# Kernel optimization log

Hardware: AMD Instinct MI355X
Metric: run time of the kernel (lower is better)

## Reference

```python
import jax, jax.numpy as jnp
import numpy as np

EPS = 1e-6          # numerical floor for norms / denominators (fp32-safe)
PROJ_EPS = 1e-5     # ball projection margin: max norm = 1 - PROJ_EPS


def _norm(x):
    return jnp.sqrt(jnp.maximum(jnp.sum(x * x, axis=-1, keepdims=True), EPS * EPS))


def hyp_proj(x):
    # project onto open Poincare ball of radius 1 - PROJ_EPS
    n = _norm(x)
    scale = jnp.minimum((1.0 - PROJ_EPS) / n, 1.0)
    return x * scale


def exp_map_zero(v):
    n = _norm(v)
    return jnp.tanh(n) * v / n


def log_map_zero(y):
    n = _norm(y)
    return jnp.arctanh(jnp.minimum(n, 1.0 - PROJ_EPS)) * y / n


def mobius_add(x, y):
    x2 = jnp.sum(x * x, axis=-1, keepdims=True)
    y2 = jnp.sum(y * y, axis=-1, keepdims=True)
    xy = jnp.sum(x * y, axis=-1, keepdims=True)
    num = (1.0 + 2.0 * xy + y2) * x + (1.0 - x2) * y
    den = 1.0 + 2.0 * xy + x2 * y2
    return num / jnp.maximum(den, EPS)


def gcn_layer(x, rows, cols, vals, W, b, n_nodes, use_act):
    # tangent-space linear transform
    pre = log_map_zero(x)                      # [N, d]
    h = pre @ W                                # [N, d]
    # sparse adjacency matmul: agg[r] += val * h[c]
    msg = vals[:, None] * h[cols]              # [E, d]
    agg = jax.ops.segment_sum(msg, rows, num_segments=n_nodes)
    out = hyp_proj(exp_map_zero(agg))
    # hyperbolic bias via mobius addition
    bh = hyp_proj(exp_map_zero(b[None, :]))    # [1, d]
    out = hyp_proj(mobius_add(out, bh))
    if use_act:
        out = hyp_proj(exp_map_zero(jnp.tanh(log_map_zero(out))))
    return out


def setup_inputs() -> dict:
    key = jax.random.key(0)
    N, D, E = 100000, 64, 3200000
    ks = jax.random.split(key, 8)
    x = jax.random.normal(ks[0], (N, D), dtype=jnp.float32) * 0.1
    edge_vals = jax.random.uniform(ks[1], (E,), dtype=jnp.float32)
    W1 = jax.random.normal(ks[2], (D, D), dtype=jnp.float32) * (1.0 / np.sqrt(D))
    b1 = jnp.zeros((D,), dtype=jnp.float32)
    W2 = jax.random.normal(ks[3], (D, D), dtype=jnp.float32) * (1.0 / np.sqrt(D))
    b2 = jnp.zeros((D,), dtype=jnp.float32)
    edge_rows = jax.random.randint(ks[4], (E,), 0, N, dtype=jnp.int64 if jax.config.jax_enable_x64 else jnp.int32).astype(jnp.int32)
    edge_cols = jax.random.randint(ks[5], (E,), 0, N, dtype=jnp.int32)
    return {"x": x, "edge_vals": edge_vals, "W1": W1, "b1": b1,
            "W2": W2, "b2": b2, "edge_rows": edge_rows, "edge_cols": edge_cols}


def reference(x, edge_vals, W1, b1, W2, b2, edge_rows, edge_cols):
    n_nodes = x.shape[0]
    # HyperKA._graph_convolution: project base embeddings, then layers with
    # mobius residual; last layer has no activation.
    e0 = hyp_proj(x)
    h1 = gcn_layer(e0, edge_rows, edge_cols, edge_vals, W1, b1, n_nodes, use_act=True)
    h1 = hyp_proj(mobius_add(h1, e0))
    h2 = gcn_layer(h1, edge_rows, edge_cols, edge_vals, W2, b2, n_nodes, use_act=False)
    h2 = hyp_proj(mobius_add(h2, h1))
    return h2
```

## Files before the change

### kernel.cpp

```cpp
#include <hip/hip_runtime.h>
#include <math.h>

#define D 64
#define EPSF 1e-6f
#define EPS2F 1e-12f
#define PROJ_EPSF 1e-5f
#define EPB 16384

typedef _Float16 f16;
typedef f16 f16x4 __attribute__((ext_vector_type(4)));
typedef f16 f16x8 __attribute__((ext_vector_type(8)));
typedef float f32x4 __attribute__((ext_vector_type(4)));

__device__ __forceinline__ float frcp(float x)  { return __builtin_amdgcn_rcpf(x); }
__device__ __forceinline__ float fsqrt(float x) { return __builtin_amdgcn_sqrtf(x); }
__device__ __forceinline__ float ftanh(float x) {
    float e = __expf(2.0f * x);
    return (e - 1.0f) * frcp(e + 1.0f);
}
__device__ __forceinline__ float fatanh(float z) {
    return 0.5f * __logf((1.0f + z) * frcp(1.0f - z));
}

__device__ __forceinline__ float wave_sum(float v) {
#pragma unroll
    for (int o = 32; o > 0; o >>= 1) v += __shfl_xor(v, o, 64);
    return v;
}
__device__ __forceinline__ float qsum(float v) {
#pragma unroll
    for (int o = 1; o < 16; o <<= 1) v += __shfl_xor(v, o, 64);
    return v;
}

__global__ __launch_bounds__(256) void k1_hist_pre(
    const int* __restrict__ rows, const float* __restrict__ x,
    const float* __restrict__ b1, const float* __restrict__ b2,
    int* __restrict__ histT, f16* __restrict__ pre,
    float* __restrict__ nbuf, float* __restrict__ bhbuf,
    int E, int N, int nb1, int NBIN)
{
    const int bid = blockIdx.x, tid = threadIdx.x;
    const int lane = tid & 63;
    if (bid < nb1) {
        __shared__ int lh[512];
        for (int i = tid; i < NBIN; i += 256) lh[i] = 0;
        __syncthreads();
        const int e0 = bid * EPB;
#pragma unroll 4
        for (int k = 0; k < EPB / 256; ++k) {
            int e = e0 + k * 256 + tid;
            if (e < E) atomicAdd(&lh[__builtin_nontemporal_load(rows + e) >> 8], 1);
        }
        __syncthreads();
        for (int i = tid; i < NBIN; i += 256) histT[i * nb1 + bid] = lh[i];
    } else if (bid == nb1) {
        if (tid < 128) {
            int wsel = tid >> 6;
            const float* b = wsel ? b2 : b1;
            float bv = b[lane];
            float nb = fsqrt(fmaxf(wave_sum(bv * bv), EPS2F));
            float t = ftanh(nb);
            float v = bv * (t * frcp(nb));
            float nv = t;
            float sc = fminf((1.0f - PROJ_EPSF) * frcp(fmaxf(nv, EPSF)), 1.0f);
            v *= sc; nv = fminf(nv, 1.0f - PROJ_EPSF);
            bhbuf[wsel * 64 + lane] = v;
            if (lane == 0) bhbuf[128 + wsel] = nv;
        }
    } else {
        int node = (bid - nb1 - 1) * 4 + (tid >> 6);
        if (node >= N) return;
        float xv = x[(size_t)node * D + lane];
        float nx = fsqrt(fmaxf(wave_sum(xv * xv), EPS2F));
        float sc = fminf((1.0f - PROJ_EPSF) * frcp(nx), 1.0f);
        float e0 = xv * sc;
        float ne0 = fminf(nx, 1.0f - PROJ_EPSF);
        pre[(size_t)node * D + lane] = (f16)(e0 * (fatanh(ne0) * frcp(fmaxf(ne0, EPSF))));
        if (lane == 0) nbuf[node] = nx;
    }
}

__global__ __launch_bounds__(64) void scan_parts(int* __restrict__ part, int P)
{
    int lane = threadIdx.x;
    int carry = 0;
    for (int b = 0; b < P; b += 64) {
        int i = b + lane;
        int v = (i < P) ? part[i] : 0;
        int inc = v;
#pragma unroll
        for (int off = 1; off < 64; off <<= 1) {
            int tu = __shfl_up(inc, off, 64);
            if (lane >= off) inc += tu;
        }
        if (i < P) part[i] = inc - v + carry;
        carry += __shfl(inc, 63, 64);
    }
}

__global__ __launch_bounds__(256) void scan_apply(
    int* __restrict__ a, const int* __restrict__ part, int L)
{
    __shared__ int wbase[4];
    int t = threadIdx.x, lane = t & 63, wid = t >> 6;
    int idx0 = blockIdx.x * 1024 + t * 4;
    int v0 = 0, v1 = 0, v2 = 0, v3 = 0;
    if (idx0 < L) { int4 v = *(const int4*)(a + idx0); v0 = v.x; v1 = v.y; v2 = v.z; v3 = v.w; }
    int s = v0 + v1 + v2 + v3;
    int inc = s;
#pragma unroll
    for (int off = 1; off < 64; off <<= 1) {
        int tu = __shfl_up(inc, off, 64);
        if (lane >= off) inc += tu;
    }
    if (lane == 63) wbase[wid] = inc;
    __syncthreads();
    if (t == 0) { int acc = 0; for (int k = 0; k < 4; ++k) { int xx = wbase[k]; wbase[k] = acc; acc += xx; } }
    __syncthreads();
    int excl = part[blockIdx.x] + wbase[wid] + (inc - s);
    if (idx0 < L) {
        int4 o; o.x = excl; o.y = excl + v0; o.z = excl + v0 + v1; o.w = excl + v0 + v1 + v2;
        *(int4*)(a + idx0) = o;
    }
}

__global__ __launch_bounds__(256) void reduce_chunks(
    const int* __restrict__ src, int* __restrict__ part, int L)
{
    __shared__ int ws[4];
    const int tid = threadIdx.x, lane = tid & 63, wid4 = tid >> 6;
    int idx0 = blockIdx.x * 1024 + tid * 4;
    int s = 0;
    if (idx0 < L) { int4 v = *(const int4*)(src + idx0); s = v.x + v.y + v.z + v.w; }
    s = (int)wave_sum((float)s);
    if (lane == 0) ws[wid4] = s;
    __syncthreads();
    if (tid == 0) part[blockIdx.x] = ws[0] + ws[1] + ws[2] + ws[3];
}

__device__ __forceinline__ void gemm64_body(
    const f16* __restrict__ A, const float* __restrict__ W,
    f16* __restrict__ C, int M, int wid, int nwaves, int lane)
{
    const int m = lane & 15;
    const int quad = lane >> 4;
    f16x8 Bfr[2][4];
#pragma unroll
    for (int kt = 0; kt < 2; ++kt)
#pragma unroll
        for (int nt = 0; nt < 4; ++nt) {
            f16x8 tmp;
#pragma unroll
            for (int j = 0; j < 8; ++j)
                tmp[j] = (f16)W[(kt * 32 + quad * 8 + j) * D + nt * 16 + m];
            Bfr[kt][nt] = tmp;
        }
    const int ntile = M >> 4;
    for (int tile = wid; tile < ntile; tile += nwaves) {
        const f16* arow = A + (size_t)(tile * 16 + m) * D;
        f16x8 a0 = *(const f16x8*)(arow + quad * 8);
        f16x8 a1 = *(const f16x8*)(arow + 32 + quad * 8);
#pragma unroll
        for (int nt = 0; nt < 4; ++nt) {
            f32x4 z = {0.0f, 0.0f, 0.0f, 0.0f};
            z = __builtin_amdgcn_mfma_f32_16x16x32_f16(a0, Bfr[0][nt], z, 0, 0, 0);
            z = __builtin_amdgcn_mfma_f32_16x16x32_f16(a1, Bfr[1][nt], z, 0, 0, 0);
#pragma unroll
            for (int r = 0; r < 4; ++r)
                C[(size_t)(tile * 16 + quad * 4 + r) * D + nt * 16 + m] = (f16)z[r];
        }
    }
}

__global__ __launch_bounds__(256) void k2_reduce_gemm(
    const int* __restrict__ histT, int* __restrict__ part, int Lp, int P,
    const f16* __restrict__ A, const float* __restrict__ W,
    f16* __restrict__ C, int M)
{
    const int tid = threadIdx.x, lane = tid & 63, wid4 = tid >> 6;
    if ((int)blockIdx.x < P) {
        __shared__ int ws[4];
        int idx0 = blockIdx.x * 1024 + tid * 4;
        int s = 0;
        if (idx0 < Lp) { int4 v = *(const int4*)(histT + idx0); s = v.x + v.y + v.z + v.w; }
        s = (int)wave_sum((float)s);
        if (lane == 0) ws[wid4] = s;
        __syncthreads();
        if (tid == 0) part[blockIdx.x] = ws[0] + ws[1] + ws[2] + ws[3];
    } else {
        int wid = (blockIdx.x - P) * 4 + wid4;
        int nwaves = (gridDim.x - P) * 4;
        gemm64_body(A, W, C, M, wid, nwaves, lane);
    }
}

__global__ __launch_bounds__(512) void p1_scatter(
    const int* __restrict__ rows, const int* __restrict__ cols,
    const float* __restrict__ vals, const int* __restrict__ histT,
    unsigned int* __restrict__ pay, unsigned char* __restrict__ rloc,
    int E, int nb1, int NBIN)
{
    __shared__ unsigned int  stage[512][32];
    __shared__ unsigned char srloc[512][32];
    __shared__ int gbase[512];
    __shared__ int cnt[512];
    __shared__ int flushed[512];
    __shared__ unsigned int msk[512];

    const int bid = blockIdx.x, tid = threadIdx.x;
    {
        int i = tid;
        gbase[i] = (i < NBIN) ? histT[i * nb1 + bid] : 0;
        cnt[i] = 0; flushed[i] = 0; msk[i] = 0u;
    }
    __syncthreads();

    const int e0 = bid * EPB;
    for (int rnd = 0; rnd < EPB / 2048; ++rnd) {
        int rr[4], cc[4]; float vv[4];
#pragma unroll
        for (int u = 0; u < 4; ++u) {
            int e = e0 + rnd * 2048 + u * 512 + tid;
            bool ok = e < E;
            rr[u] = ok ? __builtin_nontemporal_load(rows + e) : -1;
            cc[u] = ok ? __builtin_nontemporal_load(cols + e) : 0;
            vv[u] = ok ? __builtin_nontemporal_load(vals + e) : 0.0f;
        }
#pragma unroll
        for (int u = 0; u < 4; ++u) {
            if (rr[u] < 0) continue;
            int bin = rr[u] >> 8;
            unsigned int q = (unsigned int)fmaf(vv[u], 32767.0f, 0.5f);
            unsigned int p = (q << 17) | (unsigned int)cc[u];
            unsigned char rl = (unsigned char)(rr[u] & 255);
            int slot = atomicAdd(&cnt[bin], 1);
            if (slot - flushed[bin] < 32) {
                stage[bin][slot & 31] = p;
                srloc[bin][slot & 31] = rl;
                atomicOr(&msk[bin], 1u << (slot & 31));
            } else {
                int gp = gbase[bin] + slot;
                pay[gp] = p;
                rloc[gp] = rl;
            }
        }
        __syncthreads();
        if (tid < NBIN) {
            const int b = tid;
            int f = flushed[b];
            int n = cnt[b];
            unsigned int m = msk[b];
            const int gb = gbase[b];
            while (n - f >= 16) {
                const int half = (f >> 4) & 1;
                const unsigned int m16 = (m >> (half * 16)) & 0xFFFFu;
                const int base = gb + f;
                const int r0 = half * 16;
                if (m16 == 0xFFFFu) {
#pragma unroll
                    for (int k2 = 0; k2 < 16; ++k2)
                        pay[base + k2] = stage[b][r0 + k2];
#pragma unroll
                    for (int k2 = 0; k2 < 16; ++k2)
                        rloc[base + k2] = srloc[b][r0 + k2];
                } else {
                    for (int k2 = 0; k2 < 16; ++k2)
                        if (m16 & (1u << k2)) {
                            pay[base + k2] = stage[b][r0 + k2];
                            rloc[base + k2] = srloc[b][r0 + k2];
                        }
                }
                m &= ~(0xFFFFu << (half * 16));
                f += 16;
            }
            flushed[b] = f;
            msk[b] = m;
        }
        __syncthreads();
    }
    if (tid < NBIN) {
        const int b = tid;
        int f = flushed[b];
        const int n = cnt[b];
        const unsigned int m = msk[b];
        const int gb = gbase[b];
        for (; f < n; ++f) {
            if (m & (1u << (f & 31))) {
                pay[gb + f] = stage[b][f & 31];
                rloc[gb + f] = srloc[b][f & 31];
            }
        }
    }
}

__global__ __launch_bounds__(256) void band_build(
    const unsigned int* __restrict__ pay, const unsigned char* __restrict__ rloc,
    const int* __restrict__ histT, int* __restrict__ rs,
    unsigned int* __restrict__ epack, int* __restrict__ dcnt,
    int E, int nb1, int NBIN, int N)
{
    __shared__ int lh[256];
    __shared__ int cur[256];
    __shared__ int dh[256];
    __shared__ int wsum[4];
    const int b = blockIdx.x, tid = threadIdx.x;
    const int lane = tid & 63, wid = tid >> 6;
    const int segstart = histT[b * nb1];
    const int segend = (b + 1 < NBIN) ? histT[(b + 1) * nb1] : E;
    lh[tid] = 0;
    dh[tid] = 0;
    __syncthreads();
    for (int j = segstart + tid; j < segend; j += 256)
        atomicAdd(&lh[rloc[j]], 1);
    __syncthreads();
    int v = lh[tid];
    int r = b * 256 + tid;
    if (r < N) atomicAdd(&dh[v > 255 ? 255 : v], 1);
    int inc = v;
#pragma unroll
    for (int off = 1; off < 64; off <<= 1) {
        int tu = __shfl_up(inc, off, 64);
        if (lane >= off) inc += tu;
    }
    if (lane == 63) wsum[wid] = inc;
    __syncthreads();
    int base = 0;
    for (int w2 = 0; w2 < wid; ++w2) base += wsum[w2];
    int excl = base + inc - v;
    cur[tid] = excl;
    if (r < N) rs[r] = segstart + excl + v;
    __syncthreads();
    dcnt[tid * NBIN + b] = dh[tid];
    for (int j = segstart + tid; j < segend; j += 256) {
        int pos = segstart + atomicAdd(&cur[rloc[j]], 1);
        epack[pos] = pay[j];
    }
}

__global__ __launch_bounds__(256) void perm_build(
    const int* __restrict__ rs, const int* __restrict__ dcnt,
    int* __restrict__ perm, int NBIN, int N)
{
    __shared__ int cur[256];
    const int b = blockIdx.x, tid = threadIdx.x;
    cur[tid] = dcnt[tid * NBIN + b];
    __syncthreads();
    int r = b * 256 + tid;
    if (r < N) {
        int d = rs[r] - (r ? rs[r - 1] : 0);
        if (d > 255) d = 255;
        int pos = atomicAdd(&cur[d], 1);
        perm[pos] = r;
    }
}

__device__ __forceinline__ void csr_accum4(
    const int* __restrict__ rs, const unsigned int* __restrict__ epack,
    const f16* __restrict__ h, int row, int li, int qbase, float* a)
{
    const int start = (row == 0) ? 0 : rs[row - 1];
    const int end = rs[row];
    int nbat = (end - start + 15) >> 4;
#pragma unroll
    for (int o = 16; o < 64; o <<= 1) {
        int nbo = __shfl_xor(nbat, o, 64);
        nbat = nbo > nbat ? nbo : nbat;
    }
    const f16x4* __restrict__ h4 = (const f16x4*)h;
    float A0[4] = {0.f, 0.f, 0.f, 0.f}, A1[4] = {0.f, 0.f, 0.f, 0.f};
    int j = start + li;
    unsigned int p = (j < end) ? epack[j] : 0u;
    for (int bb = 0; bb < nbat; ++bb) {
        int c = (int)(p & 131071u);
        float vf = (float)(p >> 17) * (1.0f / 32767.0f);
        int jn = j + 16;
        unsigned int pn = (jn < end) ? epack[jn] : 0u;
#pragma unroll
        for (int t = 0; t < 16; t += 4) {
            int   c0 = __shfl(c,  qbase + t,     64);
            float v0 = __shfl(vf, qbase + t,     64);
            int   c1 = __shfl(c,  qbase + t + 1, 64);
            float v1 = __shfl(vf, qbase + t + 1, 64);
            int   c2 = __shfl(c,  qbase + t + 2, 64);
            float v2 = __shfl(vf, qbase + t + 2, 64);
            int   c3 = __shfl(c,  qbase + t + 3, 64);
            float v3 = __shfl(vf, qbase + t + 3, 64);
            f16x4 h0 = h4[(size_t)c0 * 16 + li];
            f16x4 h1 = h4[(size_t)c1 * 16 + li];
            f16x4 h2 = h4[(size_t)c2 * 16 + li];
            f16x4 h3 = h4[(size_t)c3 * 16 + li];
#pragma unroll
            for (int k = 0; k < 4; ++k) {
                A0[k] = fmaf(v0, (float)h0[k], A0[k]);
                A1[k] = fmaf(v1, (float)h1[k], A1[k]);
                A0[k] = fmaf(v2, (float)h2[k], A0[k]);
                A1[k] = fmaf(v3, (float)h3[k], A1[k]);
            }
        }
        j = jn; p = pn;
    }
#pragma unroll
    for (int k = 0; k < 4; ++k) a[k] = A0[k] + A1[k];
}

__global__ __launch_bounds__(256) void layer1_fused(
    const int* __restrict__ rs, const unsigned int* __restrict__ epack,
    const f16* __restrict__ h, const float* __restrict__ x,
    const float* __restrict__ bhbuf, float* __restrict__ nbuf,
    const float* __restrict__ W2, const int* __restrict__ perm,
    f16* __restrict__ h1_out, f16* __restrict__ h2lin, int N)
{
    __shared__ f16 ptile[16 * 72];
    __shared__ f16 w2l[D * D];
    __shared__ int rowids[16];

    const int tid = threadIdx.x;
    const int lane = tid & 63;
    const int q = lane >> 4, li = lane & 15, qbase = q << 4;
    const int rb = (tid >> 6) * 4 + q;
    int prow = blockIdx.x * 16 + rb;
    if (prow >= N) prow = N - 1;
    const int row = perm[prow];

    {
        const float4* W4 = (const float4*)W2;
        int i = tid;
#pragma unroll
        for (int it = 0; it < 4; ++it, i += 256) {
            float4 v4 = W4[i];
            f16x4 c4 = {(f16)v4.x, (f16)v4.y, (f16)v4.z, (f16)v4.w};
            *(f16x4*)&w2l[i * 4] = c4;
        }
    }

    float a[4];
    csr_accum4(rs, epack, h, row, li, qbase, a);

    float na = fsqrt(fmaxf(qsum(a[0]*a[0] + a[1]*a[1] + a[2]*a[2] + a[3]*a[3]), EPS2F));
    float t = ftanh(na);
    float s = t * frcp(na);
    float o[4];
#pragma unroll
    for (int k = 0; k < 4; ++k) o[k] = a[k] * s;
    float no = t;
    float sc = fminf((1.0f - PROJ_EPSF) * frcp(fmaxf(no, EPSF)), 1.0f);
#pragma unroll
    for (int k = 0; k < 4; ++k) o[k] *= sc;
    no = fminf(no, 1.0f - PROJ_EPSF);

    float4 bp4 = ((const float4*)bhbuf)[li];
    float bh[4] = {bp4.x, bp4.y, bp4.z, bp4.w};
    float nbh = bhbuf[128];
    float xy = qsum(o[0]*bh[0] + o[1]*bh[1] + o[2]*bh[2] + o[3]*bh[3]);
    float x2 = no * no, y2 = nbh * nbh;
    float rd = frcp(fmaxf(1.0f + 2.0f * xy + x2 * y2, EPSF));
    float al = (1.0f + 2.0f * xy + y2) * rd;
    float be = (1.0f - x2) * rd;
    float m[4];
#pragma unroll
    for (int k = 0; k < 4; ++k) m[k] = al * o[k] + be * bh[k];
    float nm = fsqrt(fmaxf(al*al*x2 + be*be*y2 + 2.0f*al*be*xy, EPS2F));
    sc = fminf((1.0f - PROJ_EPSF) * frcp(fmaxf(nm, EPSF)), 1.0f);
#pragma unroll
    for (int k = 0; k < 4; ++k) m[k] *= sc;
    nm = fminf(nm, 1.0f - PROJ_EPSF);

    float lg = fatanh(nm) * frcp(fmaxf(nm, EPSF));
    float w[4];
#pragma unroll
    for (int k = 0; k < 4; ++k) w[k] = ftanh(m[k] * lg);
    float nw = fsqrt(fmaxf(qsum(w[0]*w[0] + w[1]*w[1] + w[2]*w[2] + w[3]*w[3]), EPS2F));
    float tw = ftanh(nw);
    s = tw * frcp(nw);
    float ov[4];
#pragma unroll
    for (int k = 0; k < 4; ++k) ov[k] = w[k] * s;
    float nov = tw;
    sc = fminf((1.0f - PROJ_EPSF) * frcp(fmaxf(nov, EPSF)), 1.0f);
#pragma unroll
    for (int k = 0; k < 4; ++k) ov[k] *= sc;
    nov = fminf(nov, 1.0f - PROJ_EPSF);

    float4 xp4 = ((const float4*)(x + (size_t)row * D))[li];
    float xp[4] = {xp4.x, xp4.y, xp4.z, xp4.w};
    float nx = nbuf[row];
    float sce = fminf((1.0f - PROJ_EPSF) * frcp(nx), 1.0f);
    float e0[4];
#pragma unroll
    for (int k = 0; k < 4; ++k) e0[k] = xp[k] * sce;
    float ne0 = fminf(nx, 1.0f - PROJ_EPSF);
    float xy2 = qsum(ov[0]*e0[0] + ov[1]*e0[1] + ov[2]*e0[2] + ov[3]*e0[3]);
    x2 = nov * nov; y2 = ne0 * ne0;
    rd = frcp(fmaxf(1.0f + 2.0f * xy2 + x2 * y2, EPSF));
    al = (1.0f + 2.0f * xy2 + y2) * rd;
    be = (1.0f - x2) * rd;
    float h1v[4];
#pragma unroll
    for (int k = 0; k < 4; ++k) h1v[k] = al * ov[k] + be * e0[k];
    float nh = fsqrt(fmaxf(al*al*x2 + be*be*y2 + 2.0f*al*be*xy2, EPS2F));
    sc = fminf((1.0f - PROJ_EPSF) * frcp(fmaxf(nh, EPSF)), 1.0f);
#pragma unroll
    for (int k = 0; k < 4; ++k) h1v[k] *= sc;
    nh = fminf(nh, 1.0f - PROJ_EPSF);

    f16x4 hp, pp;
    float lg2 = fatanh(nh) * frcp(fmaxf(nh, EPSF));
#pragma unroll
    for (int k = 0; k < 4; ++k) { hp[k] = (f16)h1v[k]; pp[k] = (f16)(h1v[k] * lg2); }
    ((f16x4*)h1_out)[(size_t)row * 16 + li] = hp;
    *(f16x4*)&ptile[rb * 72 + li * 4] = pp;
    if (li == 0) { rowids[rb] = row; nbuf[row] = nh; }
    __syncthreads();

    {
        const int wv = tid >> 6;
        f16x8 B2[2];
#pragma unroll
        for (int kt = 0; kt < 2; ++kt) {
            f16x8 tmp;
#pragma unroll
            for (int j = 0; j < 8; ++j)
                tmp[j] = w2l[(kt * 32 + q * 8 + j) * D + wv * 16 + li];
            B2[kt] = tmp;
        }
        f16x8 a0, a1;
#pragma unroll
        for (int j = 0; j < 8; ++j) {
            a0[j] = ptile[li * 72 + q * 8 + j];
            a1[j] = ptile[li * 72 + 32 + q * 8 + j];
        }
        f32x4 z = {0.0f, 0.0f, 0.0f, 0.0f};
        z = __builtin_amdgcn_mfma_f32_16x16x32_f16(a0, B2[0], z, 0, 0, 0);
        z = __builtin_amdgcn_mfma_f32_16x16x32_f16(a1, B2[1], z, 0, 0, 0);
#pragma unroll
        for (int r = 0; r < 4; ++r)
            h2lin[(size_t)rowids[q * 4 + r] * D + wv * 16 + li] = (f16)z[r];
    }
}

__global__ __launch_bounds__(256) void layer2_fused(
    const int* __restrict__ rs, const unsigned int* __restrict__ epack,
    const f16* __restrict__ h2lin, const float* __restrict__ bhbuf,
    const float* __restrict__ nbuf, const int* __restrict__ perm,
    f16* __restrict__ h1_inout, int N)
{
    const int tid = threadIdx.x;
    const int lane = tid & 63;
    const int q = lane >> 4, li = lane & 15, qbase = q << 4;
    const int rb = (tid >> 6) * 4 + q;
    int prow = blockIdx.x * 16 + rb;
    if (prow >= N) prow = N - 1;
    const int row = perm[prow];

    float a[4];
    csr_accum4(rs, epack, h2lin, row, li, qbase, a);

    float na = fsqrt(fmaxf(qsum(a[0]*a[0] + a[1]*a[1] + a[2]*a[2] + a[3]*a[3]), EPS2F));
    float t = ftanh(na);
    float s = t * frcp(na);
    float o[4];
#pragma unroll
    for (int k = 0; k < 4; ++k) o[k] = a[k] * s;
    float no = t;
    float sc = fminf((1.0f - PROJ_EPSF) * frcp(fmaxf(no, EPSF)), 1.0f);
#pragma unroll
    for (int k = 0; k < 4; ++k) o[k] *= sc;
    no = fminf(no, 1.0f - PROJ_EPSF);

    float4 bp4 = ((const float4*)(bhbuf + 64))[li];
    float bh[4] = {bp4.x, bp4.y, bp4.z, bp4.w};
    float nbh = bhbuf[129];
    float xy = qsum(o[0]*bh[0] + o[1]*bh[1] + o[2]*bh[2] + o[3]*bh[3]);
    float x2 = no * no, y2 = nbh * nbh;
    float rd = frcp(fmaxf(1.0f + 2.0f * xy + x2 * y2, EPSF));
    float al = (1.0f + 2.0f * xy + y2) * rd;
    float be = (1.0f - x2) * rd;
    float m[4];
#pragma unroll
    for (int k = 0; k < 4; ++k) m[k] = al * o[k] + be * bh[k];
    float nm = fsqrt(fmaxf(al*al*x2 + be*be*y2 + 2.0f*al*be*xy, EPS2F));
    sc = fminf((1.0f - PROJ_EPSF) * frcp(fmaxf(nm, EPSF)), 1.0f);
#pragma unroll
    for (int k = 0; k < 4; ++k) m[k] *= sc;
    nm = fminf(nm, 1.0f - PROJ_EPSF);

    f16x4 hp = ((const f16x4*)h1_inout)[(size_t)row * 16 + li];
    float h1v[4] = {(float)hp[0], (float)hp[1], (float)hp[2], (float)hp[3]};
    float nh = nbuf[row];
    float xy2 = qsum(m[0]*h1v[0] + m[1]*h1v[1] + m[2]*h1v[2] + m[3]*h1v[3]);
    x2 = nm * nm; y2 = nh * nh;
    rd = frcp(fmaxf(1.0f + 2.0f * xy2 + x2 * y2, EPSF));
    al = (1.0f + 2.0f * xy2 + y2) * rd;
    be = (1.0f - x2) * rd;
    float r[4];
#pragma unroll
    for (int k = 0; k < 4; ++k) r[k] = al * m[k] + be * h1v[k];
    float n2 = fsqrt(fmaxf(al*al*x2 + be*be*y2 + 2.0f*al*be*xy2, EPS2F));
    sc = fminf((1.0f - PROJ_EPSF) * frcp(fmaxf(n2, EPSF)), 1.0f);
    f16x4 op;
#pragma unroll
    for (int k = 0; k < 4; ++k) op[k] = (f16)(r[k] * sc);
    ((f16x4*)h1_inout)[(size_t)row * 16 + li] = op;
}

__global__ __launch_bounds__(256) void expand4(
    const f16* __restrict__ src, float* __restrict__ dst, int n4)
{
    int i = blockIdx.x * 256 + threadIdx.x;
    if (i < n4) {
        f16x4 v = ((const f16x4*)src)[i];
        float4 o; o.x = (float)v[0]; o.y = (float)v[1]; o.z = (float)v[2]; o.w = (float)v[3];
        ((float4*)dst)[i] = o;
    }
}

extern "C" void kernel_launch(void* const* d_in, const int* in_sizes, int n_in,
                              void* d_out, int out_size, void* d_ws, size_t ws_size,
                              hipStream_t stream) {
    const float* x    = (const float*)d_in[0];
    const float* vals = (const float*)d_in[1];
    const float* W1   = (const float*)d_in[2];
    const float* b1   = (const float*)d_in[3];
    const float* W2   = (const float*)d_in[4];
    const float* b2   = (const float*)d_in[5];
    const int* rows   = (const int*)d_in[6];
    const int* cols   = (const int*)d_in[7];
    float* out = (float*)d_out;

    const int N = in_sizes[0] / D;
    const int E = in_sizes[1];
    const size_t nd = (size_t)N * D;

    const int NBIN = (N + 255) >> 8;
    const int nb1  = (E + EPB - 1) / EPB;
    const int L    = NBIN * nb1;
    const int Lp   = ((L + 1023) / 1024) * 1024;
    const int P    = Lp / 1024;

    const int L2   = 256 * NBIN;
    const int Lp2  = ((L2 + 1023) / 1024) * 1024;
    const int P2   = Lp2 / 1024;

    char* w = (char*)d_ws;
    unsigned int*  epack = (unsigned int*)w;
    unsigned int*  pay   = (unsigned int*)(w + (size_t)E * 4);
    f16*           h1    = (f16*)(w + (size_t)E * 4);
    unsigned char* rloc  = (unsigned char*)(w + (size_t)E * 8);
    int*           histT = (int*)(w + (size_t)E * 9);
    int*           dcnt  = histT + Lp;
    size_t off = (size_t)E * 9 + (size_t)(Lp + Lp2) * 4;
    int*   part  = (int*)(w + off);            off += 1024;
    int*   rs    = (int*)(w + off);            off += (size_t)N * 4;
    float* nbuf  = (float*)(w + off);          off += (size_t)N * 4;
    float* bhbuf = (float*)(w + off);          off += 1024;
    int*   perm  = (int*)(w + off);

    f16* slot0 = (f16*)d_out;
    f16* slot1 = slot0 + nd;

    const int nbpre = (N + 3) / 4;
    const int nbq   = (N + 15) / 16;

    hipMemsetAsync(histT, 0, (size_t)(Lp + Lp2) * 4, stream);
    k1_hist_pre<<<nb1 + 1 + nbpre, 256, 0, stream>>>(
        rows, x, b1, b2, histT, slot0, nbuf, bhbuf, E, N, nb1, NBIN);
    k2_reduce_gemm<<<P + 784, 256, 0, stream>>>(histT, part, Lp, P, slot0, W1, slot1, N);
    scan_parts<<<1, 64, 0, stream>>>(part, P);
    scan_apply<<<P, 256, 0, stream>>>(histT, part, Lp);
    p1_scatter<<<nb1, 512, 0, stream>>>(rows, cols, vals, histT, pay, rloc, E, nb1, NBIN);
    band_build<<<NBIN, 256, 0, stream>>>(pay, rloc, histT, rs, epack, dcnt, E, nb1, NBIN, N);
    reduce_chunks<<<P2, 256, 0, stream>>>(dcnt, part, Lp2);
    scan_parts<<<1, 64, 0, stream>>>(part, P2);
    scan_apply<<<P2, 256, 0, stream>>>(dcnt, part, Lp2);
    perm_build<<<NBIN, 256, 0, stream>>>(rs, dcnt, perm, NBIN, N);
    layer1_fused<<<nbq, 256, 0, stream>>>(rs, epack, slot1, x, bhbuf, nbuf, W2, perm,
                                          h1, slot0, N);
    layer2_fused<<<nbq, 256, 0, stream>>>(rs, epack, slot0, bhbuf, nbuf, perm, h1, N);
    expand4<<<(int)((nd / 4 + 255) / 256), 256, 0, stream>>>(h1, out, (int)(nd / 4));
}
```

Baseline: 359.0 us.

## Process each row with 8 lanes using f16x8 gathers instead of 16 lanes

The two fused layer kernels now give each destination row to an 8-lane group, with each lane gathering 16-byte f16x8 slices, so a wave handles 8 rows and a block handles 32. This halves the per-row lane count and the shuffle and reduction overhead, and issues wider memory loads per gathered neighbor. The in-block MFMA GEMM for the next layer is reorganised for a 32-row tile with two column subtiles per wave. The degree-sorted permutation is also reversed so higher-degree rows are scheduled first. In exchange, each lane uses more registers and processes twice as many neighbor batches for the same row degree.

Result: no change. 358.0 us (-0.3%).

```diff
diff --git a/kernel.cpp b/kernel.cpp
--- a/kernel.cpp
+++ b/kernel.cpp
@@ -27,9 +27,9 @@
     for (int o = 32; o > 0; o >>= 1) v += __shfl_xor(v, o, 64);
     return v;
 }
-__device__ __forceinline__ float qsum(float v) {
-#pragma unroll
-    for (int o = 1; o < 16; o <<= 1) v += __shfl_xor(v, o, 64);
+__device__ __forceinline__ float osum(float v) {
+#pragma unroll
+    for (int o = 1; o < 8; o <<= 1) v += __shfl_xor(v, o, 64);
     return v;
 }
 
@@ -351,47 +351,48 @@
         int d = rs[r] - (r ? rs[r - 1] : 0);
         if (d > 255) d = 255;
         int pos = atomicAdd(&cur[d], 1);
-        perm[pos] = r;
-    }
-}
-
-__device__ __forceinline__ void csr_accum4(
+        perm[N - 1 - pos] = r;
+    }
+}
+
+__device__ __forceinline__ void csr_accum8(
     const int* __restrict__ rs, const unsigned int* __restrict__ epack,
-    const f16* __restrict__ h, int row, int li, int qbase, float* a)
+    const f16* __restrict__ h, int row, int oli, int obase, float* a)
 {
     const int start = (row == 0) ? 0 : rs[row - 1];
     const int end = rs[row];
-    int nbat = (end - start + 15) >> 4;
-#pragma unroll
-    for (int o = 16; o < 64; o <<= 1) {
+    int nbat = (end - start + 7) >> 3;
+#pragma unroll
+    for (int o = 8; o < 64; o <<= 1) {
         int nbo = __shfl_xor(nbat, o, 64);
         nbat = nbo > nbat ? nbo : nbat;
     }
-    const f16x4* __restrict__ h4 = (const f16x4*)h;
-    float A0[4] = {0.f, 0.f, 0.f, 0.f}, A1[4] = {0.f, 0.f, 0.f, 0.f};
-    int j = start + li;
+    const f16x8* __restrict__ h8 = (const f16x8*)h;
+    float A0[8] = {0.f,0.f,0.f,0.f,0.f,0.f,0.f,0.f};
+    float A1[8] = {0.f,0.f,0.f,0.f,0.f,0.f,0.f,0.f};
+    int j = start + oli;
     unsigned int p = (j < end) ? epack[j] : 0u;
     for (int bb = 0; bb < nbat; ++bb) {
         int c = (int)(p & 131071u);
         float vf = (float)(p >> 17) * (1.0f / 32767.0f);
-        int jn = j + 16;
+        int jn = j + 8;
         unsigned int pn = (jn < end) ? epack[jn] : 0u;
 #pragma unroll
-        for (int t = 0; t < 16; t += 4) {
-            int   c0 = __shfl(c,  qbase + t,     64);
-            float v0 = __shfl(vf, qbase + t,     64);
-            int   c1 = __shfl(c,  qbase + t + 1, 64);
-            float v1 = __shfl(vf, qbase + t + 1, 64);
-            int   c2 = __shfl(c,  qbase + t + 2, 64);
-            float v2 = __shfl(vf, qbase + t + 2, 64);
-            int   c3 = __shfl(c,  qbase + t + 3, 64);
-            float v3 = __shfl(vf, qbase + t + 3, 64);
-            f16x4 h0 = h4[(size_t)c0 * 16 + li];
-            f16x4 h1 = h4[(size_t)c1 * 16 + li];
-            f16x4 h2 = h4[(size_t)c2 * 16 + li];
-            f16x4 h3 = h4[(size_t)c3 * 16 + li];
-#pragma unroll
-            for (int k = 0; k < 4; ++k) {
+        for (int t = 0; t < 8; t += 4) {
+            int   c0 = __shfl(c,  obase + t,     64);
+            float v0 = __shfl(vf, obase + t,     64);
+            int   c1 = __shfl(c,  obase + t + 1, 64);
+            float v1 = __shfl(vf, obase + t + 1, 64);
+            int   c2 = __shfl(c,  obase + t + 2, 64);
+            float v2 = __shfl(vf, obase + t + 2, 64);
+            int   c3 = __shfl(c,  obase + t + 3, 64);
+            float v3 = __shfl(vf, obase + t + 3, 64);
+            f16x8 h0 = h8[(size_t)c0 * 8 + oli];
+            f16x8 h1 = h8[(size_t)c1 * 8 + oli];
+            f16x8 h2 = h8[(size_t)c2 * 8 + oli];
+            f16x8 h3 = h8[(size_t)c3 * 8 + oli];
+#pragma unroll
+            for (int k = 0; k < 8; ++k) {
                 A0[k] = fmaf(v0, (float)h0[k], A0[k]);
                 A1[k] = fmaf(v1, (float)h1[k], A1[k]);
                 A0[k] = fmaf(v2, (float)h2[k], A0[k]);
@@ -401,7 +402,7 @@
         j = jn; p = pn;
     }
 #pragma unroll
-    for (int k = 0; k < 4; ++k) a[k] = A0[k] + A1[k];
+    for (int k = 0; k < 8; ++k) a[k] = A0[k] + A1[k];
 }
 
 __global__ __launch_bounds__(256) void layer1_fused(
@@ -411,15 +412,15 @@
     const float* __restrict__ W2, const int* __restrict__ perm,
     f16* __restrict__ h1_out, f16* __restrict__ h2lin, int N)
 {
-    __shared__ f16 ptile[16 * 72];
+    __shared__ f16 ptile[32 * 72];
     __shared__ f16 w2l[D * D];
-    __shared__ int rowids[16];
+    __shared__ int rowids[32];
 
     const int tid = threadIdx.x;
     const int lane = tid & 63;
-    const int q = lane >> 4, li = lane & 15, qbase = q << 4;
-    const int rb = (tid >> 6) * 4 + q;
-    int prow = blockIdx.x * 16 + rb;
+    const int oct = lane >> 3, oli = lane & 7, obase = lane & ~7;
+    const int rb = (tid >> 6) * 8 + oct;
+    int prow = blockIdx.x * 32 + rb;
     if (prow >= N) prow = N - 1;
     const int row = perm[prow];
 
@@ -434,108 +435,131 @@
         }
     }
 
-    float a[4];
-    csr_accum4(rs, epack, h, row, li, qbase, a);
-
-    float na = fsqrt(fmaxf(qsum(a[0]*a[0] + a[1]*a[1] + a[2]*a[2] + a[3]*a[3]), EPS2F));
+    float a[8];
+    csr_accum8(rs, epack, h, row, oli, obase, a);
+
+    float ss = 0.f;
+#pragma unroll
+    for (int k = 0; k < 8; ++k) ss += a[k] * a[k];
+    float na = fsqrt(fmaxf(osum(ss), EPS2F));
     float t = ftanh(na);
     float s = t * frcp(na);
-    float o[4];
-#pragma unroll
-    for (int k = 0; k < 4; ++k) o[k] = a[k] * s;
+    float o[8];
+#pragma unroll
+    for (int k = 0; k < 8; ++k) o[k] = a[k] * s;
     float no = t;
     float sc = fminf((1.0f - PROJ_EPSF) * frcp(fmaxf(no, EPSF)), 1.0f);
 #pragma unroll
-    for (int k = 0; k < 4; ++k) o[k] *= sc;
+    for (int k = 0; k < 8; ++k) o[k] *= sc;
     no = fminf(no, 1.0f - PROJ_EPSF);
 
-    float4 bp4 = ((const float4*)bhbuf)[li];
-    float bh[4] = {bp4.x, bp4.y, bp4.z, bp4.w};
+    float4 bpa = ((const float4*)bhbuf)[oli * 2];
+    float4 bpb = ((const float4*)bhbuf)[oli * 2 + 1];
+    float bh[8] = {bpa.x, bpa.y, bpa.z, bpa.w, bpb.x, bpb.y, bpb.z, bpb.w};
     float nbh = bhbuf[128];
-    float xy = qsum(o[0]*bh[0] + o[1]*bh[1] + o[2]*bh[2] + o[3]*bh[3]);
+    float xyp = 0.f;
+#pragma unroll
+    for (int k = 0; k < 8; ++k) xyp += o[k] * bh[k];
+    float xy = osum(xyp);
     float x2 = no * no, y2 = nbh * nbh;
     float rd = frcp(fmaxf(1.0f + 2.0f * xy + x2 * y2, EPSF));
     float al = (1.0f + 2.0f * xy + y2) * rd;
     float be = (1.0f - x2) * rd;
-    float m[4];
-#pragma unroll
-    for (int k = 0; k < 4; ++k) m[k] = al * o[k] + be * bh[k];
+    float m[8];
+#pragma unroll
+    for (int k = 0; k < 8; ++k) m[k] = al * o[k] + be * bh[k];
     float nm = fsqrt(fmaxf(al*al*x2 + be*be*y2 + 2.0f*al*be*xy, EPS2F));
     sc = fminf((1.0f - PROJ_EPSF) * frcp(fmaxf(nm, EPSF)), 1.0f);
 #pragma unroll
-    for (int k = 0; k < 4; ++k) m[k] *= sc;
+    for (int k = 0; k < 8; ++k) m[k] *= sc;
     nm = fminf(nm, 1.0f - PROJ_EPSF);
 
     float lg = fatanh(nm) * frcp(fmaxf(nm, EPSF));
-    float w[4];
-#pragma unroll
-    for (int k = 0; k < 4; ++k) w[k] = ftanh(m[k] * lg);
-    float nw = fsqrt(fmaxf(qsum(w[0]*w[0] + w[1]*w[1] + w[2]*w[2] + w[3]*w[3]), EPS2F));
+    float w[8];
+#pragma unroll
+    for (int k = 0; k < 8; ++k) w[k] = ftanh(m[k] * lg);
+    float ws = 0.f;
+#pragma unroll
+    for (int k = 0; k < 8; ++k) ws += w[k] * w[k];
+    float nw = fsqrt(fmaxf(osum(ws), EPS2F));
     float tw = ftanh(nw);
     s = tw * frcp(nw);
-    float ov[4];
-#pragma unroll
-    for (int k = 0; k < 4; ++k) ov[k] = w[k] * s;
+    float ov[8];
+#pragma unroll
+    for (int k = 0; k < 8; ++k) ov[k] = w[k] * s;
     float nov = tw;
     sc = fminf((1.0f - PROJ_EPSF) * frcp(fmaxf(nov, EPSF)), 1.0f);
 #pragma unroll
-    for (int k = 0; k < 4; ++k) ov[k] *= sc;
+    for (int k = 0; k < 8; ++k) ov[k] *= sc;
     nov = fminf(nov, 1.0f - PROJ_EPSF);
 
-    float4 xp4 = ((const float4*)(x + (size_t)row * D))[li];
-    float xp[4] = {xp4.x, xp4.y, xp4.z, xp4.w};
+    float4 xpa = ((const float4*)(x + (size_t)row * D))[oli * 2];
+    float4 xpb = ((const float4*)(x + (size_t)row * D))[oli * 2 + 1];
+    float xp[8] = {xpa.x, xpa.y, xpa.z, xpa.w, xpb.x, xpb.y, xpb.z, xpb.w};
     float nx = nbuf[row];
     float sce = fminf((1.0f - PROJ_EPSF) * frcp(nx), 1.0f);
-    float e0[4];
-#pragma unroll
-    for (int k = 0; k < 4; ++k) e0[k] = xp[k] * sce;
+    float e0[8];
+#pragma unroll
+    for (int k = 0; k < 8; ++k) e0[k] = xp[k] * sce;
     float ne0 = fminf(nx, 1.0f - PROJ_EPSF);
-    float xy2 = qsum(ov[0]*e0[0] + ov[1]*e0[1] + ov[2]*e0[2] + ov[3]*e0[3]);
-    x2 = nov * nov; y2 = ne0 * ne0;
-    rd = frcp(fmaxf(1.0f + 2.0f * xy2 + x2 * y2, EPSF));
-    al = (1.0f + 2.0f * xy2 + y2) * rd;
+    float x2p = 0.f;
+#pragma unroll
+    for (int k = 0; k < 8; ++k) x2p += ov[k] * e0[k];
+    float xy2 = osum(x2p);
+    x2 = nov * nov; float y2b = ne0 * ne0;
+    rd = frcp(fmaxf(1.0f + 2.0f * xy2 + x2 * y2b, EPSF));
+    al = (1.0f + 2.0f * xy2 + y2b) * rd;
     be = (1.0f - x2) * rd;
-    float h1v[4];
-#pragma unroll
-    for (int k = 0; k < 4; ++k) h1v[k] = al * ov[k] + be * e0[k];
-    float nh = fsqrt(fmaxf(al*al*x2 + be*be*y2 + 2.0f*al*be*xy2, EPS2F));
+    float h1v[8];
+#pragma unroll
+    for (int k = 0; k < 8; ++k) h1v[k] = al * ov[k] + be * e0[k];
+    float nh = fsqrt(fmaxf(al*al*x2 + be*be*y2b + 2.0f*al*be*xy2, EPS2F));
     sc = fminf((1.0f - PROJ_EPSF) * frcp(fmaxf(nh, EPSF)), 1.0f);
 #pragma unroll
-    for (int k = 0; k < 4; ++k) h1v[k] *= sc;
+    for (int k = 0; k < 8; ++k) h1v[k] *= sc;
     nh = fminf(nh, 1.0f - PROJ_EPSF);
 
-    f16x4 hp, pp;
+    f16x8 hp, pp;
     float lg2 = fatanh(nh) * frcp(fmaxf(nh, EPSF));
 #pragma unroll
-    for (int k = 0; k < 4; ++k) { hp[k] = (f16)h1v[k]; pp[k] = (f16)(h1v[k] * lg2); }
-    ((f16x4*)h1_out)[(size_t)row * 16 + li] = hp;
-    *(f16x4*)&ptile[rb * 72 + li * 4] = pp;
-    if (li == 0) { rowids[rb] = row; nbuf[row] = nh; }
+    for (int k = 0; k < 8; ++k) { hp[k] = (f16)h1v[k]; pp[k] = (f16)(h1v[k] * lg2); }
+    ((f16x8*)h1_out)[(size_t)row * 8 + oli] = hp;
+    *(f16x8*)&ptile[rb * 72 + oli * 8] = pp;
+    if (oli == 0) { rowids[rb] = row; nbuf[row] = nh; }
     __syncthreads();
 
     {
         const int wv = tid >> 6;
-        f16x8 B2[2];
-#pragma unroll
-        for (int kt = 0; kt < 2; ++kt) {
-            f16x8 tmp;
-#pragma unroll
-            for (int j = 0; j < 8; ++j)
-                tmp[j] = w2l[(kt * 32 + q * 8 + j) * D + wv * 16 + li];
-            B2[kt] = tmp;
-        }
+        const int rt = wv >> 1;
+        const int cb = (wv & 1) * 32;
+        const int mm = lane & 15, quad = lane >> 4;
+        f16x8 B2[2][2];
+#pragma unroll
+        for (int kt = 0; kt < 2; ++kt)
+#pragma unroll
+            for (int nt = 0; nt < 2; ++nt) {
+                f16x8 tmp;
+#pragma unroll
+                for (int j = 0; j < 8; ++j)
+                    tmp[j] = w2l[(kt * 32 + quad * 8 + j) * D + cb + nt * 16 + mm];
+                B2[kt][nt] = tmp;
+            }
         f16x8 a0, a1;
 #pragma unroll
         for (int j = 0; j < 8; ++j) {
-            a0[j] = ptile[li * 72 + q * 8 + j];
-            a1[j] = ptile[li * 72 + 32 + q * 8 + j];
-        }
-        f32x4 z = {0.0f, 0.0f, 0.0f, 0.0f};
-        z = __builtin_amdgcn_mfma_f32_16x16x32_f16(a0, B2[0], z, 0, 0, 0);
-        z = __builtin_amdgcn_mfma_f32_16x16x32_f16(a1, B2[1], z, 0, 0, 0);
-#pragma unroll
-        for (int r = 0; r < 4; ++r)
-            h2lin[(size_t)rowids[q * 4 + r] * D + wv * 16 + li] = (f16)z[r];
+            a0[j] = ptile[(rt * 16 + mm) * 72 + quad * 8 + j];
+            a1[j] = ptile[(rt * 16 + mm) * 72 + 32 + quad * 8 + j];
+        }
+#pragma unroll
+        for (int nt = 0; nt < 2; ++nt) {
+            f32x4 z = {0.0f, 0.0f, 0.0f, 0.0f};
+            z = __builtin_amdgcn_mfma_f32_16x16x32_f16(a0, B2[0][nt], z, 0, 0, 0);
+            z = __builtin_amdgcn_mfma_f32_16x16x32_f16(a1, B2[1][nt], z, 0, 0, 0);
+#pragma unroll
+            for (int r = 0; r < 4; ++r)
+                h2lin[(size_t)rowids[rt * 16 + quad * 4 + r] * D + cb + nt * 16 + mm]
+                    = (f16)z[r];
+        }
     }
 }
 
@@ -547,61 +571,73 @@
 {
     const int tid = threadIdx.x;
     const int lane = tid & 63;
-    const int q = lane >> 4, li = lane & 15, qbase = q << 4;
-    const int rb = (tid >> 6) * 4 + q;
-    int prow = blockIdx.x * 16 + rb;
+    const int oct = lane >> 3, oli = lane & 7, obase = lane & ~7;
+    const int rb = (tid >> 6) * 8 + oct;
+    int prow = blockIdx.x * 32 + rb;
     if (prow >= N) prow = N - 1;
     const int row = perm[prow];
 
-    float a[4];
-    csr_accum4(rs, epack, h2lin, row, li, qbase, a);
-
-    float na = fsqrt(fmaxf(qsum(a[0]*a[0] + a[1]*a[1] + a[2]*a[2] + a[3]*a[3]), EPS2F));
+    float a[8];
+    csr_accum8(rs, epack, h2lin, row, oli, obase, a);
+
+    float ss = 0.f;
+#pragma unroll
+    for (int k = 0; k < 8; ++k) ss += a[k] * a[k];
+    float na = fsqrt(fmaxf(osum(ss), EPS2F));
     float t = ftanh(na);
     float s = t * frcp(na);
-    float o[4];
-#pragma unroll
-    for (int k = 0; k < 4; ++k) o[k] = a[k] * s;
+    float o[8];
+#pragma unroll
+    for (int k = 0; k < 8; ++k) o[k] = a[k] * s;
     float no = t;
     float sc = fminf((1.0f - PROJ_EPSF) * frcp(fmaxf(no, EPSF)), 1.0f);
 #pragma unroll
-    for (int k = 0; k < 4; ++k) o[k] *= sc;
+    for (int k = 0; k < 8; ++k) o[k] *= sc;
     no = fminf(no, 1.0f - PROJ_EPSF);
 
-    float4 bp4 = ((const float4*)(bhbuf + 64))[li];
-    float bh[4] = {bp4.x, bp4.y, bp4.z, bp4.w};
+    float4 bpa = ((const float4*)(bhbuf + 64))[oli * 2];
+    float4 bpb = ((const float4*)(bhbuf + 64))[oli * 2 + 1];
+    float bh[8] = {bpa.x, bpa.y, bpa.z, bpa.w, bpb.x, bpb.y, bpb.z, bpb.w};
     float nbh = bhbuf[129];
-    float xy = qsum(o[0]*bh[0] + o[1]*bh[1] + o[2]*bh[2] + o[3]*bh[3]);
+    float xyp = 0.f;
+#pragma unroll
+    for (int k = 0; k < 8; ++k) xyp += o[k] * bh[k];
+    float xy = osum(xyp);
     float x2 = no * no, y2 = nbh * nbh;
     float rd = frcp(fmaxf(1.0f + 2.0f * xy + x2 * y2, EPSF));
     float al = (1.0f + 2.0f * xy + y2) * rd;
     float be = (1.0f - x2) * rd;
-    float m[4];
-#pragma unroll
-    for (int k = 0; k < 4; ++k) m[k] = al * o[k] + be * bh[k];
+    float m[8];
+#pragma unroll
+    for (int k = 0; k < 8; ++k) m[k] = al * o[k] + be * bh[k];
     float nm = fsqrt(fmaxf(al*al*x2 + be*be*y2 + 2.0f*al*be*xy, EPS2F));
     sc = fminf((1.0f - PROJ_EPSF) * frcp(fmaxf(nm, EPSF)), 1.0f);
 #pragma unroll
-    for (int k = 0; k < 4; ++k) m[k] *= sc;
+    for (int k = 0; k < 8; ++k) m[k] *= sc;
     nm = fminf(nm, 1.0f - PROJ_EPSF);
 
-    f16x4 hp = ((const f16x4*)h1_inout)[(size_t)row * 16 + li];
-    float h1v[4] = {(float)hp[0], (float)hp[1], (float)hp[2], (float)hp[3]};
+    f16x8 hp = ((const f16x8*)h1_inout)[(size_t)row * 8 + oli];
+    float h1v[8];
+#pragma unroll
+    for (int k = 0; k < 8; ++k) h1v[k] = (float)hp[k];
     float nh = nbuf[row];
-    float xy2 = qsum(m[0]*h1v[0] + m[1]*h1v[1] + m[2]*h1v[2] + m[3]*h1v[3]);
-    x2 = nm * nm; y2 = nh * nh;
-    rd = frcp(fmaxf(1.0f + 2.0f * xy2 + x2 * y2, EPSF));
-    al = (1.0f + 2.0f * xy2 + y2) * rd;
+    float x2p = 0.f;
+#pragma unroll
+    for (int k = 0; k < 8; ++k) x2p += m[k] * h1v[k];
+    float xy2 = osum(x2p);
+    x2 = nm * nm; float y2b = nh * nh;
+    rd = frcp(fmaxf(1.0f + 2.0f * xy2 + x2 * y2b, EPSF));
+    al = (1.0f + 2.0f * xy2 + y2b) * rd;
     be = (1.0f - x2) * rd;
-    float r[4];
-#pragma unroll
-    for (int k = 0; k < 4; ++k) r[k] = al * m[k] + be * h1v[k];
-    float n2 = fsqrt(fmaxf(al*al*x2 + be*be*y2 + 2.0f*al*be*xy2, EPS2F));
+    float r[8];
+#pragma unroll
+    for (int k = 0; k < 8; ++k) r[k] = al * m[k] + be * h1v[k];
+    float n2 = fsqrt(fmaxf(al*al*x2 + be*be*y2b + 2.0f*al*be*xy2, EPS2F));
     sc = fminf((1.0f - PROJ_EPSF) * frcp(fmaxf(n2, EPSF)), 1.0f);
-    f16x4 op;
-#pragma unroll
-    for (int k = 0; k < 4; ++k) op[k] = (f16)(r[k] * sc);
-    ((f16x4*)h1_inout)[(size_t)row * 16 + li] = op;
+    f16x8 op;
+#pragma unroll
+    for (int k = 0; k < 8; ++k) op[k] = (f16)(r[k] * sc);
+    ((f16x8*)h1_inout)[(size_t)row * 8 + oli] = op;
 }
 
 __global__ __launch_bounds__(256) void expand4(
@@ -660,7 +696,7 @@
     f16* slot1 = slot0 + nd;
 
     const int nbpre = (N + 3) / 4;
-    const int nbq   = (N + 15) / 16;
+    const int nbq   = (N + 31) / 32;
 
     hipMemsetAsync(histT, 0, (size_t)(Lp + Lp2) * 4, stream);
     k1_hist_pre<<<nb1 + 1 + nbpre, 256, 0, stream>>>(
```
